# Kernel optimization log

Hardware: AMD Instinct MI355X
Metric: run time of the kernel (lower is better)

Reference implementation:

```python
import jax, jax.numpy as jnp
import numpy as np

EPS = 1e-5
TOP_K = 2

def _conv(x, w, pad):
    # x: [B,Cin,H,W], w: [Cout,Cin,kh,kw]
    return jax.lax.conv_general_dilated(
        x, w, (1, 1), [(pad, pad), (pad, pad)],
        dimension_numbers=('NCHW', 'OIHW', 'NCHW'))

def _bn_eval(x, scale, bias):
    # BatchNorm2d in eval mode with running_mean=0, running_var=1
    inv = scale / jnp.sqrt(1.0 + EPS)
    return x * inv[None, :, None, None] + bias[None, :, None, None]

def setup_inputs() -> dict:
    key = jax.random.key(0)
    ks = jax.random.split(key, 8)
    B, C, O, H, W, E, HID = 16, 256, 256, 56, 56, 8, 512  # HID = int(2.0 * C)
    g = lambda k, shape, f: jax.random.normal(k, shape, jnp.float32) * f
    return {
        'x': jax.random.normal(ks[0], (B, C, H, W), jnp.float32),
        # EfficientSpatialRouter: global-avg-pool -> 1x1 conv to E logits
        'router_w': g(ks[1], (E, C), 0.01),
        'router_b': jnp.zeros((E,), jnp.float32),
        # shared expert: 1x1 conv -> BN -> SiLU
        'shared_w': g(ks[2], (O, C, 1, 1), 0.05),
        'shared_scale': jnp.ones((O,), jnp.float32),
        'shared_bias': jnp.zeros((O,), jnp.float32),
        # SimpleExpert per expert: conv3x3 C->HID, BN, SiLU, conv1x1 HID->O, BN
        'w1': g(ks[3], (E, HID, C, 3, 3), 0.02),
        'bn1_scale': jnp.ones((E, HID), jnp.float32),
        'bn1_bias': jnp.zeros((E, HID), jnp.float32),
        'w2': g(ks[4], (E, O, HID, 1, 1), 0.02),
        'bn2_scale': jnp.ones((E, O), jnp.float32),
        'bn2_bias': jnp.zeros((E, O), jnp.float32),
    }

def reference(x, router_w, router_b, shared_w, shared_scale, shared_bias,
              w1, bn1_scale, bn1_bias, w2, bn2_scale, bn2_bias):
    E = router_w.shape[0]
    # --- routing: pooled features -> logits -> softmax -> top-k renormalized ---
    pooled = x.mean(axis=(2, 3))                          # [B,C]
    logits = pooled @ router_w.T + router_b               # [B,E]
    probs = jax.nn.softmax(logits, axis=-1)
    topk_vals, topk_idx = jax.lax.top_k(probs, TOP_K)     # [B,K]
    weights = topk_vals / topk_vals.sum(axis=-1, keepdims=True)
    # --- shared expert ---
    shared = jax.nn.silu(_bn_eval(_conv(x, shared_w, 0), shared_scale, shared_bias))
    # --- expert dispatch/combine (dense-masked equivalent of gather + index_add) ---
    expert_out = jnp.zeros_like(shared)
    for e in range(E):  # fixed small expert count
        gate = jnp.sum(weights * (topk_idx == e), axis=-1)  # [B], 0 if not routed
        h = jax.nn.silu(_bn_eval(_conv(x, w1[e], 1), bn1_scale[e], bn1_bias[e]))
        y = _bn_eval(_conv(h, w2[e], 0), bn2_scale[e], bn2_bias[e])
        expert_out = expert_out + gate[:, None, None, None] * y
    # residual since in_channels == out_channels
    return shared + expert_out + x
```

## Files before the change

kernel.cpp:

```cpp
#include <hip/hip_runtime.h>
#include <hip/hip_bf16.h>

#define B_ 16
#define C_ 256
#define O_ 256
#define P_ 3136
#define E_ 8
#define HID_ 512
#define EPS_ 1e-5f

typedef __attribute__((ext_vector_type(8))) short bf16x8;
typedef __attribute__((ext_vector_type(4))) float f32x4;
typedef __hip_bfloat16 bf16;

__device__ __forceinline__ void gl2lds16(const bf16* g, bf16* l) {
  __builtin_amdgcn_global_load_lds((const __attribute__((address_space(1))) void*)g,
                                   (__attribute__((address_space(3))) void*)l,
                                   16, 0, 0);
}

__global__ __launch_bounds__(256) void xT_kernel(const float* __restrict__ x,
                                                 bf16* __restrict__ xT) {
  __shared__ float tile[64][65];
  const int p0 = blockIdx.x * 64, c0 = blockIdx.y * 64, b = blockIdx.z;
  const int t = threadIdx.x;
#pragma unroll
  for (int j = 0; j < 16; ++j) {
    int idx = t + j * 256;
    int cl = idx >> 6, pl = idx & 63;
    tile[cl][pl] = x[(size_t)(b * C_ + c0 + cl) * P_ + p0 + pl];
  }
  __syncthreads();
#pragma unroll
  for (int j = 0; j < 16; ++j) {
    int idx = t + j * 256;
    int pl = idx >> 6, cl = idx & 63;
    xT[(size_t)(b * P_ + p0 + pl) * C_ + c0 + cl] = __float2bfloat16(tile[cl][pl]);
  }
}

__global__ __launch_bounds__(256) void w1cvt_kernel(const float* __restrict__ w1,
                                                    const float* __restrict__ bn1_scale,
                                                    bf16* __restrict__ w1b) {
  const int eh = blockIdx.x;
  const int e = eh >> 9, hid = eh & 511;
  __shared__ float buf[2304];
  const float* src = w1 + (size_t)eh * 2304;
  const int t = threadIdx.x;
  for (int i = t; i < 2304; i += 256) buf[i] = src[i];
  __syncthreads();
  const float inv = bn1_scale[eh] * (1.0f / sqrtf(1.0f + EPS_));
  for (int i = t; i < 2304; i += 256) {
    int rs = i >> 8, c = i & 255;
    w1b[((size_t)(e * 9 + rs) * HID_ + hid) * C_ + c] = __float2bfloat16(buf[c * 9 + rs] * inv);
  }
}

__global__ __launch_bounds__(256) void w2cvt_kernel(const float* __restrict__ w2,
                                                    const float* __restrict__ bn2_scale,
                                                    bf16* __restrict__ w2b) {
  const int i = blockIdx.x * 256 + threadIdx.x;
  const int eo = i >> 9;
  w2b[i] = __float2bfloat16(w2[i] * (bn2_scale[eo] * (1.0f / sqrtf(1.0f + EPS_))));
}

__global__ __launch_bounds__(256) void wshcvt_kernel(const float* __restrict__ wsh,
                                                     const float* __restrict__ sscale,
                                                     bf16* __restrict__ wshb) {
  const int i = blockIdx.x * 256 + threadIdx.x;
  wshb[i] = __float2bfloat16(wsh[i] * (sscale[i >> 8] * (1.0f / sqrtf(1.0f + EPS_))));
}

__global__ __launch_bounds__(256) void pooled_kernel(const float* __restrict__ x,
                                                     float* __restrict__ pooled) {
  const int row = blockIdx.x;
  const float* p = x + (size_t)row * P_;
  float s = 0.f;
  for (int i = threadIdx.x; i < P_; i += 256) s += p[i];
#pragma unroll
  for (int off = 32; off; off >>= 1) s += __shfl_down(s, off);
  __shared__ float ws4[4];
  if ((threadIdx.x & 63) == 0) ws4[threadIdx.x >> 6] = s;
  __syncthreads();
  if (threadIdx.x == 0) pooled[row] = (ws4[0] + ws4[1] + ws4[2] + ws4[3]) * (1.0f / P_);
}

__global__ __launch_bounds__(256) void router_kernel(const float* __restrict__ pooled,
                                                     const float* __restrict__ rw,
                                                     const float* __restrict__ rb,
                                                     const float* __restrict__ bn2_bias,
                                                     int* __restrict__ ridx,
                                                     float* __restrict__ rwt,
                                                     float* __restrict__ bsum) {
  __shared__ float lp[B_ * C_];
  __shared__ float llog[B_ * E_];
  __shared__ int lidx[B_ * 2];
  __shared__ float lw[B_ * 2];
  const int t = threadIdx.x;
  for (int i = t; i < B_ * C_; i += 256) lp[i] = pooled[i];
  __syncthreads();
  if (t < B_ * E_) {
    int b = t >> 3, e = t & 7;
    float s = rb[e];
    for (int c = 0; c < C_; ++c) s += lp[b * C_ + c] * rw[e * C_ + c];
    llog[t] = s;
  }
  __syncthreads();
  if (t < B_) {
    float pr[E_];
    float m = -1e30f;
    for (int e = 0; e < E_; ++e) { pr[e] = llog[t * E_ + e]; m = fmaxf(m, pr[e]); }
    float s = 0.f;
    for (int e = 0; e < E_; ++e) { pr[e] = __expf(pr[e] - m); s += pr[e]; }
    const float is = 1.f / s;
    for (int e = 0; e < E_; ++e) pr[e] *= is;
    int i0 = 0; float v0 = pr[0];
    for (int e = 1; e < E_; ++e) if (pr[e] > v0) { v0 = pr[e]; i0 = e; }
    int i1 = -1; float v1 = -1.f;
    for (int e = 0; e < E_; ++e) if (e != i0 && pr[e] > v1) { v1 = pr[e]; i1 = e; }
    const float wsum = 1.f / (v0 + v1);
    ridx[t * 2] = i0; ridx[t * 2 + 1] = i1;
    rwt[t * 2] = v0 * wsum; rwt[t * 2 + 1] = v1 * wsum;
    lidx[t * 2] = i0; lidx[t * 2 + 1] = i1;
    lw[t * 2] = v0 * wsum; lw[t * 2 + 1] = v1 * wsum;
  }
  __syncthreads();
  for (int i = t; i < B_ * O_; i += 256) {
    int b = i >> 8, o = i & 255;
    bsum[i] = lw[b * 2] * bn2_bias[lidx[b * 2] * O_ + o]
            + lw[b * 2 + 1] * bn2_bias[lidx[b * 2 + 1] * O_ + o];
  }
}

__global__ __launch_bounds__(256) void conv1_kernel(
    const bf16* __restrict__ xT, const bf16* __restrict__ w1b,
    const float* __restrict__ bn1_bias, const int* __restrict__ ridx,
    const float* __restrict__ rwt, const bf16* __restrict__ zp,
    bf16* __restrict__ h) {
  __shared__ __align__(16) bf16 ldsA[112 * 32];
  __shared__ __align__(16) bf16 ldsB[128 * 32];
  const int t = threadIdx.x;
  const int p0 = blockIdx.x * 112;
  const int h0 = blockIdx.y * 128;
  const int bs = blockIdx.z;
  const int b = bs >> 1;
  const int e = ridx[bs];
  const float wk = rwt[bs];

  const int lane = t & 63, wv = t >> 6;
  const int koff = (lane >> 4) * 8;
  const int r16 = lane & 15;

  const int rA0 = t >> 2;
  const int rA1 = rA0 + 64;
  const int cA = (t & 3) * 8;
  const int pA0 = p0 + rA0;
  const int pA1 = p0 + rA1;
  const int yA0 = pA0 / 56, xA0 = pA0 % 56;
  const int yA1 = pA1 / 56, xA1 = pA1 % 56;

  f32x4 acc[7][2] = {};

  for (int rs = 0; rs < 9; ++rs) {
    const int dr = rs / 3 - 1, ds = rs % 3 - 1;
    const int off = dr * 56 + ds;
    const bool v0 = ((unsigned)(yA0 + dr) < 56u) & ((unsigned)(xA0 + ds) < 56u);
    const bool v1 = ((unsigned)(yA1 + dr) < 56u) & ((unsigned)(xA1 + ds) < 56u);
    const bf16* sA0 = v0 ? xT + (size_t)(b * P_ + pA0 + off) * C_ + cA : zp + cA;
    const bf16* sA1 = v1 ? xT + (size_t)(b * P_ + pA1 + off) * C_ + cA : zp + cA;
    const bf16* sB = w1b + (size_t)((e * 9 + rs) * HID_ + h0 + rA0) * C_ + cA;

    for (int c0 = 0; c0 < C_; c0 += 32) {
      gl2lds16(sA0 + c0, ldsA + t * 8);
      if (t < 192) gl2lds16(sA1 + c0, ldsA + (t + 256) * 8);
      gl2lds16(sB + c0, ldsB + t * 8);
      gl2lds16(sB + 64 * C_ + c0, ldsB + (t + 256) * 8);
      __syncthreads();
      bf16x8 bf0 = *(const bf16x8*)(ldsB + (wv * 32 + r16) * 32 + koff);
      bf16x8 bf1 = *(const bf16x8*)(ldsB + (wv * 32 + 16 + r16) * 32 + koff);
#pragma unroll
      for (int mi = 0; mi < 7; ++mi) {
        bf16x8 af = *(const bf16x8*)(ldsA + (mi * 16 + r16) * 32 + koff);
        acc[mi][0] = __builtin_amdgcn_mfma_f32_16x16x32_bf16(af, bf0, acc[mi][0], 0, 0, 0);
        acc[mi][1] = __builtin_amdgcn_mfma_f32_16x16x32_bf16(af, bf1, acc[mi][1], 0, 0, 0);
      }
      __syncthreads();
    }
  }

  const int rowq = (lane >> 4) * 4;
#pragma unroll
  for (int ni = 0; ni < 2; ++ni) {
    const int hid = h0 + wv * 32 + ni * 16 + r16;
    const float bias = bn1_bias[e * HID_ + hid];
#pragma unroll
    for (int mi = 0; mi < 7; ++mi) {
#pragma unroll
      for (int i = 0; i < 4; ++i) {
        const int p = p0 + mi * 16 + rowq + i;
        float v = acc[mi][ni][i] + bias;
        v = v / (1.f + __expf(-v));
        h[((size_t)bs * P_ + p) * HID_ + hid] = __float2bfloat16(wk * v);
      }
    }
  }
}

__global__ __launch_bounds__(256) void combine_kernel(
    const bf16* __restrict__ xT, const bf16* __restrict__ h,
    const bf16* __restrict__ wshb, const bf16* __restrict__ w2b,
    const float* __restrict__ sbias, const float* __restrict__ bsum,
    const int* __restrict__ ridx, const float* __restrict__ x,
    float* __restrict__ out) {
  __shared__ __align__(16) bf16 ldsA[128 * 32];
  __shared__ __align__(16) bf16 ldsB[112 * 32];
  const int t = threadIdx.x;
  const int p0 = blockIdx.x * 112;
  const int o0 = blockIdx.y * 128;
  const int b = blockIdx.z;
  const int lane = t & 63, wv = t >> 6;
  const int koff = (lane >> 4) * 8;
  const int r16 = lane & 15;
  const int rT = t >> 2;
  const int cT = (t & 3) * 8;

  f32x4 acc[2][7] = {};
  f32x4 res[2][7];

  {
    const bf16* sA = wshb + (size_t)(o0 + rT) * C_ + cT;
    const bf16* sB = xT + (size_t)(b * P_ + p0 + rT) * C_ + cT;
    for (int c0 = 0; c0 < C_; c0 += 32) {
      gl2lds16(sA + c0, ldsA + t * 8);
      gl2lds16(sA + 64 * C_ + c0, ldsA + (t + 256) * 8);
      gl2lds16(sB + c0, ldsB + t * 8);
      if (t < 192) gl2lds16(sB + 64 * C_ + c0, ldsB + (t + 256) * 8);
      __syncthreads();
      bf16x8 a0 = *(const bf16x8*)(ldsA + (wv * 32 + r16) * 32 + koff);
      bf16x8 a1 = *(const bf16x8*)(ldsA + (wv * 32 + 16 + r16) * 32 + koff);
#pragma unroll
      for (int ni = 0; ni < 7; ++ni) {
        bf16x8 bf = *(const bf16x8*)(ldsB + (ni * 16 + r16) * 32 + koff);
        acc[0][ni] = __builtin_amdgcn_mfma_f32_16x16x32_bf16(a0, bf, acc[0][ni], 0, 0, 0);
        acc[1][ni] = __builtin_amdgcn_mfma_f32_16x16x32_bf16(a1, bf, acc[1][ni], 0, 0, 0);
      }
      __syncthreads();
    }
  }
  const int rowq = (lane >> 4) * 4;
#pragma unroll
  for (int mi = 0; mi < 2; ++mi) {
    const int ob = o0 + wv * 32 + mi * 16 + rowq;
#pragma unroll
    for (int i = 0; i < 4; ++i) {
      const float bias = sbias[ob + i];
#pragma unroll
      for (int ni = 0; ni < 7; ++ni) {
        float v = acc[mi][ni][i] + bias;
        res[mi][ni][i] = v / (1.f + __expf(-v));
        acc[mi][ni][i] = 0.f;
      }
    }
  }
  for (int slot = 0; slot < 2; ++slot) {
    const int e = ridx[b * 2 + slot];
    const bf16* sA = w2b + (size_t)(e * O_ + o0 + rT) * HID_ + cT;
    const bf16* sB = h + (size_t)((b * 2 + slot) * P_ + p0 + rT) * HID_ + cT;
    for (int c0 = 0; c0 < HID_; c0 += 32) {
      gl2lds16(sA + c0, ldsA + t * 8);
      gl2lds16(sA + 64 * HID_ + c0, ldsA + (t + 256) * 8);
      gl2lds16(sB + c0, ldsB + t * 8);
      if (t < 192) gl2lds16(sB + 64 * HID_ + c0, ldsB + (t + 256) * 8);
      __syncthreads();
      bf16x8 a0 = *(const bf16x8*)(ldsA + (wv * 32 + r16) * 32 + koff);
      bf16x8 a1 = *(const bf16x8*)(ldsA + (wv * 32 + 16 + r16) * 32 + koff);
#pragma unroll
      for (int ni = 0; ni < 7; ++ni) {
        bf16x8 bf = *(const bf16x8*)(ldsB + (ni * 16 + r16) * 32 + koff);
        acc[0][ni] = __builtin_amdgcn_mfma_f32_16x16x32_bf16(a0, bf, acc[0][ni], 0, 0, 0);
        acc[1][ni] = __builtin_amdgcn_mfma_f32_16x16x32_bf16(a1, bf, acc[1][ni], 0, 0, 0);
      }
      __syncthreads();
    }
  }
#pragma unroll
  for (int mi = 0; mi < 2; ++mi) {
    const int ob = o0 + wv * 32 + mi * 16 + rowq;
#pragma unroll
    for (int i = 0; i < 4; ++i) {
      const int o = ob + i;
      const float bb = bsum[b * O_ + o];
      const size_t orow = (size_t)(b * O_ + o) * P_;
#pragma unroll
      for (int ni = 0; ni < 7; ++ni) {
        const int p = p0 + ni * 16 + r16;
        out[orow + p] = res[mi][ni][i] + acc[mi][ni][i] + bb + x[orow + p];
      }
    }
  }
}

constexpr size_t SZ_XT = (size_t)B_ * P_ * C_ * 2;
constexpr size_t SZ_W1B = (size_t)E_ * 9 * HID_ * C_ * 2;
constexpr size_t SZ_W2B = (size_t)E_ * O_ * HID_ * 2;
constexpr size_t SZ_WSHB = (size_t)O_ * C_ * 2;
constexpr size_t SZ_POOL = (size_t)B_ * C_ * 4;
constexpr size_t SZ_BSUM = (size_t)B_ * O_ * 4;
constexpr size_t SZ_H = (size_t)B_ * 2 * P_ * HID_ * 2;

constexpr size_t OFF_XT = 0;
constexpr size_t OFF_W1B = OFF_XT + SZ_XT;
constexpr size_t OFF_W2B = OFF_W1B + SZ_W1B;
constexpr size_t OFF_WSHB = OFF_W2B + SZ_W2B;
constexpr size_t OFF_POOL = OFF_WSHB + SZ_WSHB;
constexpr size_t OFF_RIDX = OFF_POOL + SZ_POOL;
constexpr size_t OFF_RWT = OFF_RIDX + 128;
constexpr size_t OFF_BSUM = OFF_RWT + 128;
constexpr size_t OFF_ZERO = OFF_BSUM + SZ_BSUM;
constexpr size_t OFF_H = OFF_ZERO + 1024;

extern "C" void kernel_launch(void* const* d_in, const int* in_sizes, int n_in,
                              void* d_out, int out_size, void* d_ws, size_t ws_size,
                              hipStream_t stream) {
  const float* x = (const float*)d_in[0];
  const float* router_w = (const float*)d_in[1];
  const float* router_b = (const float*)d_in[2];
  const float* shared_w = (const float*)d_in[3];
  const float* shared_scale = (const float*)d_in[4];
  const float* shared_bias = (const float*)d_in[5];
  const float* w1 = (const float*)d_in[6];
  const float* bn1_scale = (const float*)d_in[7];
  const float* bn1_bias = (const float*)d_in[8];
  const float* w2 = (const float*)d_in[9];
  const float* bn2_scale = (const float*)d_in[10];
  const float* bn2_bias = (const float*)d_in[11];
  float* out = (float*)d_out;
  char* ws = (char*)d_ws;

  bf16* xT = (bf16*)(ws + OFF_XT);
  bf16* w1b = (bf16*)(ws + OFF_W1B);
  bf16* w2b = (bf16*)(ws + OFF_W2B);
  bf16* wshb = (bf16*)(ws + OFF_WSHB);
  float* pooled = (float*)(ws + OFF_POOL);
  int* ridx = (int*)(ws + OFF_RIDX);
  float* rwt = (float*)(ws + OFF_RWT);
  float* bsum = (float*)(ws + OFF_BSUM);
  bf16* zp = (bf16*)(ws + OFF_ZERO);
  bf16* h = (bf16*)(ws + OFF_H);

  hipMemsetAsync(ws + OFF_ZERO, 0, 1024, stream);

  xT_kernel<<<dim3(49, 4, 16), 256, 0, stream>>>(x, xT);
  w1cvt_kernel<<<E_ * HID_, 256, 0, stream>>>(w1, bn1_scale, w1b);
  w2cvt_kernel<<<(E_ * O_ * HID_) / 256, 256, 0, stream>>>(w2, bn2_scale, w2b);
  wshcvt_kernel<<<(O_ * C_) / 256, 256, 0, stream>>>(shared_w, shared_scale, wshb);
  pooled_kernel<<<B_ * C_, 256, 0, stream>>>(x, pooled);
  router_kernel<<<1, 256, 0, stream>>>(pooled, router_w, router_b, bn2_bias, ridx, rwt, bsum);
  conv1_kernel<<<dim3(28, 4, 32), 256, 0, stream>>>(xT, w1b, bn1_bias, ridx, rwt, zp, h);
  combine_kernel<<<dim3(28, 2, 16), 256, 0, stream>>>(xT, h, wshb, w2b, shared_bias, bsum, ridx, x, out);
}
```

Measured before the change: 612.2 us.

## Double-buffer GEMM kernels with 128x128 tiles, swizzled LDS, and fuse pooling into transpose

Both MFMA kernels (conv1 implicit GEMM and combine) move to 128x128 tiles with a 2x2 wave layout and double-buffered LDS. The next K-slice is prefetched while the current one computes, and a single barrier is used per step. An XOR swizzle on the LDS k-slots is meant to cut bank conflicts, and s_setprio wraps the MFMA bursts. The combine kernel now runs the shared and expert GEMMs in one pipelined loop, reusing the accumulators after applying SiLU at the switch point. The separate pooling kernel is removed; the transpose kernel accumulates channel means with atomics into a zeroed buffer, which adds atomic traffic and non-deterministic summation order, and the partial tile rows at the spatial edge are handled with a zero page and bounds checks.

```diff
diff --git a/kernel.cpp b/kernel.cpp
--- a/kernel.cpp
+++ b/kernel.cpp
@@ -20,7 +20,8 @@
 }
 
 __global__ __launch_bounds__(256) void xT_kernel(const float* __restrict__ x,
-                                                 bf16* __restrict__ xT) {
+                                                 bf16* __restrict__ xT,
+                                                 float* __restrict__ pooled) {
   __shared__ float tile[64][65];
   const int p0 = blockIdx.x * 64, c0 = blockIdx.y * 64, b = blockIdx.z;
   const int t = threadIdx.x;
@@ -36,6 +37,12 @@
     int idx = t + j * 256;
     int pl = idx >> 6, cl = idx & 63;
     xT[(size_t)(b * P_ + p0 + pl) * C_ + c0 + cl] = __float2bfloat16(tile[cl][pl]);
+  }
+  if (t < 64) {
+    float s = 0.f;
+#pragma unroll 8
+    for (int pl = 0; pl < 64; ++pl) s += tile[t][pl];
+    atomicAdd(&pooled[b * C_ + c0 + t], s * (1.0f / P_));
   }
 }
 
@@ -69,20 +76,6 @@
                                                      bf16* __restrict__ wshb) {
   const int i = blockIdx.x * 256 + threadIdx.x;
   wshb[i] = __float2bfloat16(wsh[i] * (sscale[i >> 8] * (1.0f / sqrtf(1.0f + EPS_))));
-}
-
-__global__ __launch_bounds__(256) void pooled_kernel(const float* __restrict__ x,
-                                                     float* __restrict__ pooled) {
-  const int row = blockIdx.x;
-  const float* p = x + (size_t)row * P_;
-  float s = 0.f;
-  for (int i = threadIdx.x; i < P_; i += 256) s += p[i];
-#pragma unroll
-  for (int off = 32; off; off >>= 1) s += __shfl_down(s, off);
-  __shared__ float ws4[4];
-  if ((threadIdx.x & 63) == 0) ws4[threadIdx.x >> 6] = s;
-  __syncthreads();
-  if (threadIdx.x == 0) pooled[row] = (ws4[0] + ws4[1] + ws4[2] + ws4[3]) * (1.0f / P_);
 }
 
 __global__ __launch_bounds__(256) void router_kernel(const float* __restrict__ pooled,
@@ -137,10 +130,10 @@
     const float* __restrict__ bn1_bias, const int* __restrict__ ridx,
     const float* __restrict__ rwt, const bf16* __restrict__ zp,
     bf16* __restrict__ h) {
-  __shared__ __align__(16) bf16 ldsA[112 * 32];
-  __shared__ __align__(16) bf16 ldsB[128 * 32];
-  const int t = threadIdx.x;
-  const int p0 = blockIdx.x * 112;
+  __shared__ __align__(16) bf16 ldsA[2][128 * 32];
+  __shared__ __align__(16) bf16 ldsB[2][128 * 32];
+  const int t = threadIdx.x;
+  const int p0 = blockIdx.x * 128;
   const int h0 = blockIdx.y * 128;
   const int bs = blockIdx.z;
   const int b = bs >> 1;
@@ -148,59 +141,79 @@
   const float wk = rwt[bs];
 
   const int lane = t & 63, wv = t >> 6;
-  const int koff = (lane >> 4) * 8;
-  const int r16 = lane & 15;
-
-  const int rA0 = t >> 2;
-  const int rA1 = rA0 + 64;
-  const int cA = (t & 3) * 8;
-  const int pA0 = p0 + rA0;
-  const int pA1 = p0 + rA1;
-  const int yA0 = pA0 / 56, xA0 = pA0 % 56;
-  const int yA1 = pA1 / 56, xA1 = pA1 % 56;
-
-  f32x4 acc[7][2] = {};
-
-  for (int rs = 0; rs < 9; ++rs) {
-    const int dr = rs / 3 - 1, ds = rs % 3 - 1;
-    const int off = dr * 56 + ds;
-    const bool v0 = ((unsigned)(yA0 + dr) < 56u) & ((unsigned)(xA0 + ds) < 56u);
-    const bool v1 = ((unsigned)(yA1 + dr) < 56u) & ((unsigned)(xA1 + ds) < 56u);
-    const bf16* sA0 = v0 ? xT + (size_t)(b * P_ + pA0 + off) * C_ + cA : zp + cA;
-    const bf16* sA1 = v1 ? xT + (size_t)(b * P_ + pA1 + off) * C_ + cA : zp + cA;
-    const bf16* sB = w1b + (size_t)((e * 9 + rs) * HID_ + h0 + rA0) * C_ + cA;
-
-    for (int c0 = 0; c0 < C_; c0 += 32) {
-      gl2lds16(sA0 + c0, ldsA + t * 8);
-      if (t < 192) gl2lds16(sA1 + c0, ldsA + (t + 256) * 8);
-      gl2lds16(sB + c0, ldsB + t * 8);
-      gl2lds16(sB + 64 * C_ + c0, ldsB + (t + 256) * 8);
-      __syncthreads();
-      bf16x8 bf0 = *(const bf16x8*)(ldsB + (wv * 32 + r16) * 32 + koff);
-      bf16x8 bf1 = *(const bf16x8*)(ldsB + (wv * 32 + 16 + r16) * 32 + koff);
-#pragma unroll
-      for (int mi = 0; mi < 7; ++mi) {
-        bf16x8 af = *(const bf16x8*)(ldsA + (mi * 16 + r16) * 32 + koff);
-        acc[mi][0] = __builtin_amdgcn_mfma_f32_16x16x32_bf16(af, bf0, acc[mi][0], 0, 0, 0);
-        acc[mi][1] = __builtin_amdgcn_mfma_f32_16x16x32_bf16(af, bf1, acc[mi][1], 0, 0, 0);
-      }
-      __syncthreads();
-    }
-  }
-
-  const int rowq = (lane >> 4) * 4;
-#pragma unroll
-  for (int ni = 0; ni < 2; ++ni) {
-    const int hid = h0 + wv * 32 + ni * 16 + r16;
-    const float bias = bn1_bias[e * HID_ + hid];
-#pragma unroll
-    for (int mi = 0; mi < 7; ++mi) {
-#pragma unroll
-      for (int i = 0; i < 4; ++i) {
-        const int p = p0 + mi * 16 + rowq + i;
-        float v = acc[mi][ni][i] + bias;
-        v = v / (1.f + __expf(-v));
-        h[((size_t)bs * P_ + p) * HID_ + hid] = __float2bfloat16(wk * v);
+  const int wm = wv >> 1, wn = wv & 1;
+  const int r16 = lane & 15, q = lane >> 4;
+  const int kslot = (q ^ (r16 & 3)) * 8;
+
+  const int rA = t >> 2;
+  const int cSw = ((t & 3) ^ (rA & 3)) * 8;
+  const int pA0 = p0 + rA, pA1 = pA0 + 64;
+  const int yA0 = pA0 / 56, xA0 = pA0 - yA0 * 56;
+  const int yA1 = pA1 / 56, xA1 = pA1 - yA1 * 56;
+  const bool vP1 = (pA1 < P_);
+  const bf16* xb = xT + (size_t)b * P_ * C_ + cSw;
+  const bf16* wb = w1b + ((size_t)(e * 9) * HID_ + h0 + rA) * C_ + cSw;
+
+  f32x4 acc[4][4] = {};
+
+#define STAGE(buf, s) { \
+    const int tap_ = (s) >> 3, c0k_ = ((s) & 7) * 32; \
+    const int dr_ = tap_ / 3 - 1, dc_ = tap_ % 3 - 1; \
+    const int off_ = dr_ * 56 + dc_; \
+    const bool v0_ = ((unsigned)(yA0 + dr_) < 56u) & ((unsigned)(xA0 + dc_) < 56u); \
+    const bool v1_ = vP1 & ((unsigned)(yA1 + dr_) < 56u) & ((unsigned)(xA1 + dc_) < 56u); \
+    const bf16* a0_ = v0_ ? xb + (size_t)(pA0 + off_) * C_ + c0k_ : zp; \
+    const bf16* a1_ = v1_ ? xb + (size_t)(pA1 + off_) * C_ + c0k_ : zp; \
+    const bf16* b_ = wb + (size_t)(tap_ * HID_) * C_ + c0k_; \
+    gl2lds16(a0_, ldsA[buf] + t * 8); \
+    gl2lds16(a1_, ldsA[buf] + 2048 + t * 8); \
+    gl2lds16(b_, ldsB[buf] + t * 8); \
+    gl2lds16(b_ + 64 * C_, ldsB[buf] + 2048 + t * 8); \
+  }
+
+  STAGE(0, 0);
+  __syncthreads();
+  for (int s = 0; s < 72; ++s) {
+    const int cur = s & 1;
+    if (s < 71) STAGE(cur ^ 1, s + 1);
+    const bf16* lA = ldsA[cur];
+    const bf16* lB = ldsB[cur];
+    bf16x8 af[4], bfr[4];
+#pragma unroll
+    for (int i = 0; i < 4; ++i) {
+      af[i]  = *(const bf16x8*)(lA + (wm * 64 + i * 16 + r16) * 32 + kslot);
+      bfr[i] = *(const bf16x8*)(lB + (wn * 64 + i * 16 + r16) * 32 + kslot);
+    }
+    __builtin_amdgcn_s_setprio(1);
+#pragma unroll
+    for (int mi = 0; mi < 4; ++mi)
+#pragma unroll
+      for (int ni = 0; ni < 4; ++ni)
+        acc[mi][ni] = __builtin_amdgcn_mfma_f32_16x16x32_bf16(af[mi], bfr[ni], acc[mi][ni], 0, 0, 0);
+    __builtin_amdgcn_s_setprio(0);
+    if (s < 71) __syncthreads();
+  }
+#undef STAGE
+
+  const int rowq = q * 4;
+  float bias[4];
+#pragma unroll
+  for (int ni = 0; ni < 4; ++ni)
+    bias[ni] = bn1_bias[e * HID_ + h0 + wn * 64 + ni * 16 + r16];
+#pragma unroll
+  for (int mi = 0; mi < 4; ++mi) {
+#pragma unroll
+    for (int i = 0; i < 4; ++i) {
+      const int p = p0 + wm * 64 + mi * 16 + rowq + i;
+      if (p < P_) {
+        const size_t base = ((size_t)bs * P_ + p) * HID_;
+#pragma unroll
+        for (int ni = 0; ni < 4; ++ni) {
+          const int hid = h0 + wn * 64 + ni * 16 + r16;
+          float v = acc[mi][ni][i] + bias[ni];
+          v = v / (1.f + __expf(-v));
+          h[base + hid] = __float2bfloat16(wk * v);
+        }
       }
     }
   }
@@ -211,90 +224,98 @@
     const bf16* __restrict__ wshb, const bf16* __restrict__ w2b,
     const float* __restrict__ sbias, const float* __restrict__ bsum,
     const int* __restrict__ ridx, const float* __restrict__ x,
-    float* __restrict__ out) {
-  __shared__ __align__(16) bf16 ldsA[128 * 32];
-  __shared__ __align__(16) bf16 ldsB[112 * 32];
-  const int t = threadIdx.x;
-  const int p0 = blockIdx.x * 112;
+    const bf16* __restrict__ zp, float* __restrict__ out) {
+  __shared__ __align__(16) bf16 ldsA[2][128 * 32];
+  __shared__ __align__(16) bf16 ldsB[2][128 * 32];
+  const int t = threadIdx.x;
+  const int p0 = blockIdx.x * 128;
   const int o0 = blockIdx.y * 128;
   const int b = blockIdx.z;
+  const int e0 = ridx[b * 2], e1 = ridx[b * 2 + 1];
+
   const int lane = t & 63, wv = t >> 6;
-  const int koff = (lane >> 4) * 8;
-  const int r16 = lane & 15;
-  const int rT = t >> 2;
-  const int cT = (t & 3) * 8;
-
-  f32x4 acc[2][7] = {};
-  f32x4 res[2][7];
-
-  {
-    const bf16* sA = wshb + (size_t)(o0 + rT) * C_ + cT;
-    const bf16* sB = xT + (size_t)(b * P_ + p0 + rT) * C_ + cT;
-    for (int c0 = 0; c0 < C_; c0 += 32) {
-      gl2lds16(sA + c0, ldsA + t * 8);
-      gl2lds16(sA + 64 * C_ + c0, ldsA + (t + 256) * 8);
-      gl2lds16(sB + c0, ldsB + t * 8);
-      if (t < 192) gl2lds16(sB + 64 * C_ + c0, ldsB + (t + 256) * 8);
-      __syncthreads();
-      bf16x8 a0 = *(const bf16x8*)(ldsA + (wv * 32 + r16) * 32 + koff);
-      bf16x8 a1 = *(const bf16x8*)(ldsA + (wv * 32 + 16 + r16) * 32 + koff);
-#pragma unroll
-      for (int ni = 0; ni < 7; ++ni) {
-        bf16x8 bf = *(const bf16x8*)(ldsB + (ni * 16 + r16) * 32 + koff);
-        acc[0][ni] = __builtin_amdgcn_mfma_f32_16x16x32_bf16(a0, bf, acc[0][ni], 0, 0, 0);
-        acc[1][ni] = __builtin_amdgcn_mfma_f32_16x16x32_bf16(a1, bf, acc[1][ni], 0, 0, 0);
-      }
-      __syncthreads();
-    }
-  }
-  const int rowq = (lane >> 4) * 4;
-#pragma unroll
-  for (int mi = 0; mi < 2; ++mi) {
-    const int ob = o0 + wv * 32 + mi * 16 + rowq;
+  const int wm = wv >> 1, wn = wv & 1;
+  const int r16 = lane & 15, q = lane >> 4;
+  const int kslot = (q ^ (r16 & 3)) * 8;
+
+  const int rA = t >> 2;
+  const int cSw = ((t & 3) ^ (rA & 3)) * 8;
+  const int pB0 = p0 + rA, pB1 = pB0 + 64;
+  const bool vB1 = (pB1 < P_);
+  const bf16* shA = wshb + (size_t)(o0 + rA) * C_ + cSw;
+  const bf16* xB = xT + (size_t)b * P_ * C_ + cSw;
+
+  f32x4 acc[4][4] = {};
+
+#define CSTAGE(buf, s) { \
+    if ((s) < 8) { \
+      const int c0k_ = (s) * 32; \
+      gl2lds16(shA + c0k_, ldsA[buf] + t * 8); \
+      gl2lds16(shA + 64 * C_ + c0k_, ldsA[buf] + 2048 + t * 8); \
+      gl2lds16(xB + (size_t)pB0 * C_ + c0k_, ldsB[buf] + t * 8); \
+      gl2lds16(vB1 ? xB + (size_t)pB1 * C_ + c0k_ : zp, ldsB[buf] + 2048 + t * 8); \
+    } else { \
+      const int ss_ = (s) - 8; const int slot_ = ss_ >> 4; const int c0k_ = (ss_ & 15) * 32; \
+      const int ee_ = slot_ ? e1 : e0; \
+      const bf16* wA_ = w2b + ((size_t)(ee_ * O_) + o0 + rA) * HID_ + c0k_ + cSw; \
+      const bf16* hB_ = h + ((size_t)(b * 2 + slot_) * P_) * HID_ + c0k_ + cSw; \
+      gl2lds16(wA_, ldsA[buf] + t * 8); \
+      gl2lds16(wA_ + 64 * HID_, ldsA[buf] + 2048 + t * 8); \
+      gl2lds16(hB_ + (size_t)pB0 * HID_, ldsB[buf] + t * 8); \
+      gl2lds16(vB1 ? hB_ + (size_t)pB1 * HID_ : zp, ldsB[buf] + 2048 + t * 8); \
+    } \
+  }
+
+  CSTAGE(0, 0);
+  __syncthreads();
+  for (int s = 0; s < 40; ++s) {
+    const int cur = s & 1;
+    if (s < 39) CSTAGE(cur ^ 1, s + 1);
+    const bf16* lA = ldsA[cur];
+    const bf16* lB = ldsB[cur];
+    bf16x8 af[4], bfr[4];
 #pragma unroll
     for (int i = 0; i < 4; ++i) {
-      const float bias = sbias[ob + i];
-#pragma unroll
-      for (int ni = 0; ni < 7; ++ni) {
-        float v = acc[mi][ni][i] + bias;
-        res[mi][ni][i] = v / (1.f + __expf(-v));
-        acc[mi][ni][i] = 0.f;
-      }
-    }
-  }
-  for (int slot = 0; slot < 2; ++slot) {
-    const int e = ridx[b * 2 + slot];
-    const bf16* sA = w2b + (size_t)(e * O_ + o0 + rT) * HID_ + cT;
-    const bf16* sB = h + (size_t)((b * 2 + slot) * P_ + p0 + rT) * HID_ + cT;
-    for (int c0 = 0; c0 < HID_; c0 += 32) {
-      gl2lds16(sA + c0, ldsA + t * 8);
-      gl2lds16(sA + 64 * HID_ + c0, ldsA + (t + 256) * 8);
-      gl2lds16(sB + c0, ldsB + t * 8);
-      if (t < 192) gl2lds16(sB + 64 * HID_ + c0, ldsB + (t + 256) * 8);
-      __syncthreads();
-      bf16x8 a0 = *(const bf16x8*)(ldsA + (wv * 32 + r16) * 32 + koff);
-      bf16x8 a1 = *(const bf16x8*)(ldsA + (wv * 32 + 16 + r16) * 32 + koff);
-#pragma unroll
-      for (int ni = 0; ni < 7; ++ni) {
-        bf16x8 bf = *(const bf16x8*)(ldsB + (ni * 16 + r16) * 32 + koff);
-        acc[0][ni] = __builtin_amdgcn_mfma_f32_16x16x32_bf16(a0, bf, acc[0][ni], 0, 0, 0);
-        acc[1][ni] = __builtin_amdgcn_mfma_f32_16x16x32_bf16(a1, bf, acc[1][ni], 0, 0, 0);
-      }
-      __syncthreads();
-    }
-  }
-#pragma unroll
-  for (int mi = 0; mi < 2; ++mi) {
-    const int ob = o0 + wv * 32 + mi * 16 + rowq;
+      af[i]  = *(const bf16x8*)(lA + (wm * 64 + i * 16 + r16) * 32 + kslot);
+      bfr[i] = *(const bf16x8*)(lB + (wn * 64 + i * 16 + r16) * 32 + kslot);
+    }
+    __builtin_amdgcn_s_setprio(1);
+#pragma unroll
+    for (int mi = 0; mi < 4; ++mi)
+#pragma unroll
+      for (int ni = 0; ni < 4; ++ni)
+        acc[mi][ni] = __builtin_amdgcn_mfma_f32_16x16x32_bf16(af[mi], bfr[ni], acc[mi][ni], 0, 0, 0);
+    __builtin_amdgcn_s_setprio(0);
+    if (s == 7) {
+      const int rowq_ = q * 4;
+#pragma unroll
+      for (int mi = 0; mi < 4; ++mi)
+#pragma unroll
+        for (int i = 0; i < 4; ++i) {
+          const float bias_ = sbias[o0 + wm * 64 + mi * 16 + rowq_ + i];
+#pragma unroll
+          for (int ni = 0; ni < 4; ++ni) {
+            float v = acc[mi][ni][i] + bias_;
+            acc[mi][ni][i] = v / (1.f + __expf(-v));
+          }
+        }
+    }
+    if (s < 39) __syncthreads();
+  }
+#undef CSTAGE
+
+  const int rowq = q * 4;
+#pragma unroll
+  for (int mi = 0; mi < 4; ++mi) {
 #pragma unroll
     for (int i = 0; i < 4; ++i) {
-      const int o = ob + i;
+      const int o = o0 + wm * 64 + mi * 16 + rowq + i;
       const float bb = bsum[b * O_ + o];
       const size_t orow = (size_t)(b * O_ + o) * P_;
 #pragma unroll
-      for (int ni = 0; ni < 7; ++ni) {
-        const int p = p0 + ni * 16 + r16;
-        out[orow + p] = res[mi][ni][i] + acc[mi][ni][i] + bb + x[orow + p];
+      for (int ni = 0; ni < 4; ++ni) {
+        const int p = p0 + wn * 64 + ni * 16 + r16;
+        if (p < P_) out[orow + p] = acc[mi][ni][i] + bb + x[orow + p];
       }
     }
   }
@@ -348,14 +369,14 @@
   bf16* zp = (bf16*)(ws + OFF_ZERO);
   bf16* h = (bf16*)(ws + OFF_H);
 
+  hipMemsetAsync(ws + OFF_POOL, 0, SZ_POOL, stream);
   hipMemsetAsync(ws + OFF_ZERO, 0, 1024, stream);
 
-  xT_kernel<<<dim3(49, 4, 16), 256, 0, stream>>>(x, xT);
+  xT_kernel<<<dim3(49, 4, 16), 256, 0, stream>>>(x, xT, pooled);
   w1cvt_kernel<<<E_ * HID_, 256, 0, stream>>>(w1, bn1_scale, w1b);
   w2cvt_kernel<<<(E_ * O_ * HID_) / 256, 256, 0, stream>>>(w2, bn2_scale, w2b);
   wshcvt_kernel<<<(O_ * C_) / 256, 256, 0, stream>>>(shared_w, shared_scale, wshb);
-  pooled_kernel<<<B_ * C_, 256, 0, stream>>>(x, pooled);
   router_kernel<<<1, 256, 0, stream>>>(pooled, router_w, router_b, bn2_bias, ridx, rwt, bsum);
-  conv1_kernel<<<dim3(28, 4, 32), 256, 0, stream>>>(xT, w1b, bn1_bias, ridx, rwt, zp, h);
-  combine_kernel<<<dim3(28, 2, 16), 256, 0, stream>>>(xT, h, wshb, w2b, shared_bias, bsum, ridx, x, out);
-}
+  conv1_kernel<<<dim3(25, 4, 32), 256, 0, stream>>>(xT, w1b, bn1_bias, ridx, rwt, zp, h);
+  combine_kernel<<<dim3(25, 2, 16), 256, 0, stream>>>(xT, h, wshb, w2b, shared_bias, bsum, ridx, x, zp, out);
+}
```

Measured after the change: 675.5 us. 1.1x slower.
